# Optimization experiments

Hardware: AMD Instinct MI355X
Metric: run time of the kernel (lower is better)

## Reference

```python
import jax, jax.numpy as jnp
import numpy as np

B, N, D, K = 8, 200000, 16, 512
MAX_CP = K  # upper bound on number of condensation points per event
ATTR_W, REPL_W, BG_W = 1.0, 1.0, 2.0


def setup_inputs() -> dict:
    key = jax.random.key(0)
    k1, k2, k3 = jax.random.split(key, 3)
    beta = jax.random.normal(k1, (B, N, 1), jnp.float32)
    embed = jax.random.normal(k2, (B, N, D), jnp.float32)
    r = jax.random.randint(k3, (B, N), 0, K + 8)
    slice_id = jnp.where(r < K, r, -1).astype(jnp.int32)

    def _first_occ(sid_b):
        fg = sid_b >= 0
        seg = jnp.where(fg, sid_b, K)
        fi = jax.ops.segment_min(jnp.where(fg, jnp.arange(N), N), seg, num_segments=K + 1)[:K]
        present = fi < N
        return jnp.clip(fi, 0, N - 1), present

    fi, pres = jax.vmap(_first_occ)(slice_id)
    # exactly one condensation point per present instance (its first hit)
    is_cp = jnp.zeros((B, N), jnp.int32).at[jnp.arange(B)[:, None], fi].max(pres.astype(jnp.int32))
    return {"beta": beta, "embed": embed, "slice_id": slice_id, "is_cp": is_cp}


def _per_event(beta_b, emb_b, sid, cp):
    # beta_b:[N], emb_b:[N,D], sid:[N] int, cp:[N] int
    fg = sid >= 0
    bg = ~fg
    seg = jnp.where(fg, sid, K)            # background -> dummy segment K
    sid_c = jnp.clip(sid, 0, K - 1)
    counts = jax.ops.segment_sum(fg.astype(jnp.float32), seg, num_segments=K + 1)[:K]
    present = counts > 0
    cp_fg = (cp == 1) & fg
    cp_cnt = jax.ops.segment_sum(cp_fg.astype(jnp.float32), seg, num_segments=K + 1)[:K]
    valid = present & (cp_cnt == 1)        # instances entering the CE term

    # per-instance cross-entropy: lse(beta over instance hits) - beta[cp]
    beta_m = jnp.where(fg, beta_b, -jnp.inf)
    m = jax.ops.segment_max(beta_m, seg, num_segments=K + 1)[:K]
    m_safe = jnp.where(jnp.isfinite(m), m, 0.0)
    e = jnp.where(fg, jnp.exp(beta_b - m_safe[sid_c]), 0.0)
    sumexp = jax.ops.segment_sum(e, seg, num_segments=K + 1)[:K]
    lse = m_safe + jnp.log(jnp.maximum(sumexp, 1e-30))
    cp_beta = jax.ops.segment_sum(jnp.where(cp_fg, beta_b, 0.0), seg, num_segments=K + 1)[:K]
    ce = jnp.where(valid, lse - cp_beta, 0.0)
    slice_count = jnp.sum(valid)
    beta_loss = jnp.sum(ce) / jnp.maximum(slice_count, 1)

    # background beta penalty
    nbg = jnp.sum(bg)
    bg_mean = jnp.sum(jnp.where(bg, jax.nn.sigmoid(beta_b), 0.0)) / jnp.maximum(nbg, 1)
    beta_loss = beta_loss + jnp.where(nbg > 0, BG_W * bg_mean, 0.0)

    # attraction: per instance, mean squared distance of hits to its first cp embedding
    idx = jnp.where(cp_fg, jnp.arange(N), N)
    fi = jax.ops.segment_min(idx, seg, num_segments=K + 1)[:K]
    has_cp = present & (cp_cnt >= 1)
    cp_emb = emb_b[jnp.clip(fi, 0, N - 1)]          # [K,D]
    ref = cp_emb[sid_c]                              # [N,D] gather per hit
    d = jnp.where(fg, jnp.sum((emb_b - ref) ** 2, axis=-1), 0.0)
    dsum = jax.ops.segment_sum(d, seg, num_segments=K + 1)[:K]
    attr = ATTR_W * jnp.sum(jnp.where(has_cp, dsum / jnp.maximum(counts, 1.0), 0.0))

    # repulsion: pairwise exp(-dist^2) over ALL cp hits (diagonal included, as in torch .mean())
    cp_all = cp == 1
    ncp = jnp.sum(cp_all)
    order = jnp.argsort(jnp.where(cp_all, 0, 1))     # stable: cps first, by index
    topidx = order[:MAX_CP]
    vmask = cp_all[topidx]
    ce2 = emb_b[topidx]                               # [MAX_CP, D]
    dist2 = jnp.sum((ce2[:, None, :] - ce2[None, :, :]) ** 2, axis=-1)
    w = vmask[:, None] & vmask[None, :]
    rep_sum = jnp.sum(jnp.where(w, jnp.exp(-dist2), 0.0))
    rep = jnp.where(ncp > 1, REPL_W * rep_sum / jnp.maximum(ncp * ncp, 1), 0.0)

    loss_b = beta_loss + attr + rep
    include = slice_count > 0
    return loss_b, beta_loss, attr, rep, include


def _forward(beta, embed, slice_id, is_cp):
    loss_b, bl, al, rl, inc = jax.vmap(_per_event)(beta[..., 0], embed, slice_id, is_cp)
    incf = inc.astype(loss_b.dtype)
    count = jnp.sum(incf)
    denom = jnp.maximum(count, 1.0)
    total = jnp.where(count > 0, jnp.sum(loss_b * incf) / denom, 0.0)
    beta_log = jnp.sum(bl * incf) / denom
    attr_log = jnp.sum(al * incf) / denom
    repl_log = jnp.sum(rl * incf) / denom
    return total, beta_log, attr_log, repl_log


def reference(beta, embed, slice_id, is_cp):
    return _forward(beta, embed, slice_id, is_cp)
```

## Files before the change

kernel.cpp:

```cpp
#include <hip/hip_runtime.h>
#include <math.h>

#define Bb 8
#define Nn 200000
#define Dd 16
#define Kk 512

__global__ __launch_bounds__(256) void k_init(int* packed, float* cpb, float* se,
                                              int* fi, float* ds,
                                              int* nbg, float* sig, int* cpc, float* rep) {
  int i = blockIdx.x * 256 + threadIdx.x;
  if (i < Bb * Kk) { packed[i] = 0; cpb[i] = 0.f; se[i] = 0.f; fi[i] = Nn; ds[i] = 0.f; }
  if (i < Bb) { nbg[i] = 0; sig[i] = 0.f; cpc[i] = 0; rep[i] = 0.f; }
}

__global__ __launch_bounds__(256) void k_pass1(const float* __restrict__ beta,
                                               const int* __restrict__ sid,
                                               const int* __restrict__ cp,
                                               int* packed, float* cp_beta_g, float* sumexp_g,
                                               int* fi_g, int* nbg, float* sig,
                                               int* cp_count, int* cp_idx) {
  const int b = blockIdx.y;
  __shared__ int   s_cnt[Kk];
  __shared__ float s_cb[Kk];
  __shared__ float s_se[Kk];
  __shared__ int   s_fi[Kk];
  __shared__ int   s_nbg;
  __shared__ float s_sig;
  for (int k = threadIdx.x; k < Kk; k += 256) { s_cnt[k] = 0; s_cb[k] = 0.f; s_se[k] = 0.f; s_fi[k] = Nn; }
  if (threadIdx.x == 0) { s_nbg = 0; s_sig = 0.f; }
  __syncthreads();

  const int NV = Nn / 4;
  const int nchunks = gridDim.x;
  const int chunk = (NV + nchunks - 1) / nchunks;
  const int start = blockIdx.x * chunk;
  const int end = min(start + chunk, NV);
  const size_t base = (size_t)b * Nn;
  const int4*   sid4  = (const int4*)(sid + base);
  const int4*   cp4   = (const int4*)(cp + base);
  const float4* beta4 = (const float4*)(beta + base);

  int lnbg = 0; float lsig = 0.f;
  for (int v = start + threadIdx.x; v < end; v += 256) {
    int4 s4 = sid4[v];
    int4 c4 = cp4[v];
    float4 b4 = beta4[v];
    int ss[4] = {s4.x, s4.y, s4.z, s4.w};
    int cc[4] = {c4.x, c4.y, c4.z, c4.w};
    float bb[4] = {b4.x, b4.y, b4.z, b4.w};
    #pragma unroll
    for (int t = 0; t < 4; t++) {
      int s = ss[t], c = cc[t];
      float bv = bb[t];
      int n = v * 4 + t;
      if (s >= 0) {
        atomicAdd(&s_cnt[s], 1 + ((c == 1) ? (1 << 20) : 0));
        atomicAdd(&s_se[s], __expf(bv));
        if (c == 1) {
          atomicAdd(&s_cb[s], bv);
          atomicMin(&s_fi[s], n);
        }
      } else {
        lnbg++; lsig += 1.f / (1.f + __expf(-bv));
      }
      if (c == 1) {
        int pos = atomicAdd(&cp_count[b], 1);
        if (pos < 512) cp_idx[b * 512 + pos] = n;
      }
    }
  }
  if (lnbg) { atomicAdd(&s_nbg, lnbg); atomicAdd(&s_sig, lsig); }
  __syncthreads();

  for (int k = threadIdx.x; k < Kk; k += 256) {
    int c = s_cnt[k];
    if (c) {
      atomicAdd(&packed[b * Kk + k], c);
      atomicAdd(&sumexp_g[b * Kk + k], s_se[k]);
      float cb = s_cb[k]; if (cb != 0.f) atomicAdd(&cp_beta_g[b * Kk + k], cb);
      int f = s_fi[k];    if (f < Nn)    atomicMin(&fi_g[b * Kk + k], f);
    }
  }
  if (threadIdx.x == 0 && s_nbg) { atomicAdd(&nbg[b], s_nbg); atomicAdd(&sig[b], s_sig); }
}

__global__ __launch_bounds__(256) void k_gather(const float* __restrict__ emb,
                                                const int* __restrict__ fi_g,
                                                const int* __restrict__ cp_count,
                                                const int* __restrict__ cp_idx,
                                                float* ref_emb, float* cp_emb) {
  int i = blockIdx.x * 256 + threadIdx.x;
  const int total = Bb * Kk * Dd;
  if (i < total) {
    int b = i / (Kk * Dd);
    int rem = i % (Kk * Dd);
    int k = rem / Dd, d = rem % Dd;
    int f = fi_g[b * Kk + k]; if (f > Nn - 1) f = Nn - 1;
    ref_emb[i] = emb[((size_t)b * Nn + f) * Dd + d];
  } else {
    int j = i - total;
    if (j < Bb * 512 * Dd) {
      int b = j / (512 * Dd);
      int rem = j % (512 * Dd);
      int idx = rem / Dd, d = rem % Dd;
      int nc = cp_count[b]; if (nc > 512) nc = 512;
      if (idx < nc) {
        int n = cp_idx[b * 512 + idx];
        cp_emb[j] = emb[((size_t)b * Nn + n) * Dd + d];
      }
    }
  }
}

__global__ __launch_bounds__(256) void k_pass2(const int* __restrict__ sid,
                                               const float* __restrict__ emb,
                                               const float* __restrict__ ref_emb,
                                               float* dsum_g) {
  const int b = blockIdx.y;
  __shared__ float4 s_ref4[Kk * 5];
  __shared__ float s_d[Kk];
  {
    const float4* src = (const float4*)(ref_emb + (size_t)b * Kk * Dd);
    for (int i = threadIdx.x; i < Kk * 4; i += 256) {
      int k = i >> 2, j = i & 3;
      s_ref4[k * 5 + j] = src[i];
    }
  }
  for (int k = threadIdx.x; k < Kk; k += 256) s_d[k] = 0.f;
  __syncthreads();

  const int nchunks = gridDim.x;
  const int chunk = (Nn + nchunks - 1) / nchunks;
  const int start = blockIdx.x * chunk;
  const int end = min(start + chunk, Nn);
  const size_t base = (size_t)b * Nn;

  for (int n = start + threadIdx.x; n < end; n += 256) {
    int s = sid[base + n];
    if (s >= 0) {
      const float4* e4 = (const float4*)(emb + (base + (size_t)n) * Dd);
      float4 a0 = e4[0], a1 = e4[1], a2 = e4[2], a3 = e4[3];
      const float4* r4 = &s_ref4[s * 5];
      float4 r0 = r4[0], r1 = r4[1], r2 = r4[2], r3 = r4[3];
      float d = 0.f, df;
      df = a0.x - r0.x; d = fmaf(df, df, d);
      df = a0.y - r0.y; d = fmaf(df, df, d);
      df = a0.z - r0.z; d = fmaf(df, df, d);
      df = a0.w - r0.w; d = fmaf(df, df, d);
      df = a1.x - r1.x; d = fmaf(df, df, d);
      df = a1.y - r1.y; d = fmaf(df, df, d);
      df = a1.z - r1.z; d = fmaf(df, df, d);
      df = a1.w - r1.w; d = fmaf(df, df, d);
      df = a2.x - r2.x; d = fmaf(df, df, d);
      df = a2.y - r2.y; d = fmaf(df, df, d);
      df = a2.z - r2.z; d = fmaf(df, df, d);
      df = a2.w - r2.w; d = fmaf(df, df, d);
      df = a3.x - r3.x; d = fmaf(df, df, d);
      df = a3.y - r3.y; d = fmaf(df, df, d);
      df = a3.z - r3.z; d = fmaf(df, df, d);
      df = a3.w - r3.w; d = fmaf(df, df, d);
      atomicAdd(&s_d[s], d);
    }
  }
  __syncthreads();
  for (int k = threadIdx.x; k < Kk; k += 256) {
    float v = s_d[k];
    if (v != 0.f) atomicAdd(&dsum_g[b * Kk + k], v);
  }
}

__global__ __launch_bounds__(256) void k_rep(const float* __restrict__ cp_emb,
                                             const int* __restrict__ cp_count,
                                             float* rep_acc) {
  const int b = blockIdx.y;
  int nc = cp_count[b]; if (nc > 512) nc = 512;
  __shared__ float s_e[512 * 17];
  for (int i = threadIdx.x; i < nc * Dd; i += 256) {
    int r = i >> 4, d = i & 15;
    s_e[r * 17 + d] = cp_emb[(size_t)b * 512 * Dd + i];
  }
  __syncthreads();

  const int rows = 512 / gridDim.x;
  int i = blockIdx.x * rows + (threadIdx.x >> 3);
  int js = threadIdx.x & 7;
  float acc = 0.f;
  if (i < nc) {
    float e[16];
    #pragma unroll
    for (int d = 0; d < 16; d++) e[d] = s_e[i * 17 + d];
    for (int j = js; j < nc; j += 8) {
      const float* r = &s_e[j * 17];
      float dist = 0.f;
      #pragma unroll
      for (int d = 0; d < 16; d++) { float df = e[d] - r[d]; dist += df * df; }
      acc += __expf(-dist);
    }
  }
  __shared__ float s_red;
  if (threadIdx.x == 0) s_red = 0.f;
  __syncthreads();
  for (int off = 32; off; off >>= 1) acc += __shfl_down(acc, off, 64);
  if ((threadIdx.x & 63) == 0 && acc != 0.f) atomicAdd(&s_red, acc);
  __syncthreads();
  if (threadIdx.x == 0 && s_red != 0.f) atomicAdd(&rep_acc[b], s_red);
}

__global__ __launch_bounds__(512) void k_final(const int* __restrict__ packed,
                                               const float* __restrict__ cp_beta,
                                               const float* __restrict__ sumexp,
                                               const float* __restrict__ dsum,
                                               const int* __restrict__ nbg,
                                               const float* __restrict__ sig,
                                               const int* __restrict__ cp_count,
                                               const float* __restrict__ rep_acc,
                                               float* __restrict__ out) {
  const int b = threadIdx.x >> 6;
  const int lane = threadIdx.x & 63;
  float ce = 0.f, at = 0.f, sc = 0.f;
  #pragma unroll
  for (int i = 0; i < Kk / 64; i++) {
    int k = i * 64 + lane;
    int   pc = packed[b * Kk + k];
    float se = sumexp[b * Kk + k];
    float cb = cp_beta[b * Kk + k];
    float dv = dsum[b * Kk + k];
    int cnt = pc & 0xFFFFF;
    int cpc = pc >> 20;
    if (cnt > 0) {
      if (cpc == 1) { ce += __logf(fmaxf(se, 1e-30f)) - cb; sc += 1.f; }
      if (cpc >= 1) at += dv / (float)cnt;
    }
  }
  #pragma unroll
  for (int off = 32; off; off >>= 1) {
    ce += __shfl_down(ce, off, 64);
    at += __shfl_down(at, off, 64);
    sc += __shfl_down(sc, off, 64);
  }
  __shared__ float lb_s[Bb], bl_s[Bb], al_s[Bb], rl_s[Bb];
  __shared__ int inc_s[Bb];
  if (lane == 0) {
    int scb = (int)(sc + 0.5f);
    float bl = ce / (float)max(scb, 1);
    int nb = nbg[b];
    if (nb > 0) bl += 2.0f * sig[b] / (float)nb;
    int ncp = cp_count[b];
    float rl = (ncp > 1) ? rep_acc[b] / fmaxf((float)ncp * (float)ncp, 1.f) : 0.f;
    bl_s[b] = bl; al_s[b] = at; rl_s[b] = rl; lb_s[b] = bl + at + rl;
    inc_s[b] = (scb > 0) ? 1 : 0;
  }
  __syncthreads();
  if (threadIdx.x == 0) {
    float cnt = 0.f, st = 0.f, sb = 0.f, sa = 0.f, sr = 0.f;
    for (int b2 = 0; b2 < Bb; b2++) {
      if (inc_s[b2]) { cnt += 1.f; st += lb_s[b2]; sb += bl_s[b2]; sa += al_s[b2]; sr += rl_s[b2]; }
    }
    float denom = fmaxf(cnt, 1.f);
    out[0] = (cnt > 0.f) ? st / denom : 0.f;
    out[1] = sb / denom;
    out[2] = sa / denom;
    out[3] = sr / denom;
  }
}

extern "C" void kernel_launch(void* const* d_in, const int* in_sizes, int n_in,
                              void* d_out, int out_size, void* d_ws, size_t ws_size,
                              hipStream_t stream) {
  const float* beta = (const float*)d_in[0];
  const float* emb  = (const float*)d_in[1];
  const int*   sid  = (const int*)d_in[2];
  const int*   cp   = (const int*)d_in[3];
  float* out = (float*)d_out;

  char* ws = (char*)d_ws;
  size_t off = 0;
  auto alloc = [&](size_t bytes) -> void* {
    void* p = ws + off;
    off += (bytes + 255) & ~(size_t)255;
    return p;
  };
  int*   packed   = (int*)  alloc(Bb * Kk * sizeof(int));
  float* cp_beta  = (float*)alloc(Bb * Kk * sizeof(float));
  float* sumexp   = (float*)alloc(Bb * Kk * sizeof(float));
  int*   fi       = (int*)  alloc(Bb * Kk * sizeof(int));
  float* dsum     = (float*)alloc(Bb * Kk * sizeof(float));
  int*   nbg      = (int*)  alloc(Bb * sizeof(int));
  float* sig      = (float*)alloc(Bb * sizeof(float));
  int*   cp_count = (int*)  alloc(Bb * sizeof(int));
  float* rep_acc  = (float*)alloc(Bb * sizeof(float));
  int*   cp_idx   = (int*)  alloc(Bb * 512 * sizeof(int));
  float* ref_emb  = (float*)alloc(Bb * Kk * Dd * sizeof(float));
  float* cp_emb   = (float*)alloc(Bb * 512 * Dd * sizeof(float));

  k_init<<<(Bb * Kk + 255) / 256, 256, 0, stream>>>(packed, cp_beta, sumexp, fi, dsum,
                                                    nbg, sig, cp_count, rep_acc);
  k_pass1<<<dim3(64, Bb), 256, 0, stream>>>(beta, sid, cp, packed, cp_beta, sumexp, fi,
                                            nbg, sig, cp_count, cp_idx);
  k_gather<<<(2 * Bb * Kk * Dd + 255) / 256, 256, 0, stream>>>(emb, fi, cp_count, cp_idx,
                                                               ref_emb, cp_emb);
  k_pass2<<<dim3(128, Bb), 256, 0, stream>>>(sid, emb, ref_emb, dsum);
  k_rep<<<dim3(16, Bb), 256, 0, stream>>>(cp_emb, cp_count, rep_acc);
  k_final<<<1, 512, 0, stream>>>(packed, cp_beta, sumexp, dsum, nbg, sig,
                                 cp_count, rep_acc, out);
}
```

Baseline: 216.1 us.

## Fold gather kernel into pass2 and rep, vectorize pass2 over four points

Removes the separate gather kernel. Reference embeddings are loaded straight from emb at the first-hit indices inside pass2, and condensation-point embeddings inside k_rep, which saves one launch and the intermediate buffers. pass2 now processes four points per thread, using an int4 sid load and sixteen float4 embedding loads, with a mask in place of the branch for background points. Grid sizes also change (pass1 to 128 chunks, pass2 to 96). The shared reference array drops its padding, which may add LDS bank conflicts, and each thread now holds more registers.

```diff
diff --git a/kernel.cpp b/kernel.cpp
--- a/kernel.cpp
+++ b/kernel.cpp
@@ -85,64 +85,45 @@
   if (threadIdx.x == 0 && s_nbg) { atomicAdd(&nbg[b], s_nbg); atomicAdd(&sig[b], s_sig); }
 }
 
-__global__ __launch_bounds__(256) void k_gather(const float* __restrict__ emb,
-                                                const int* __restrict__ fi_g,
-                                                const int* __restrict__ cp_count,
-                                                const int* __restrict__ cp_idx,
-                                                float* ref_emb, float* cp_emb) {
-  int i = blockIdx.x * 256 + threadIdx.x;
-  const int total = Bb * Kk * Dd;
-  if (i < total) {
-    int b = i / (Kk * Dd);
-    int rem = i % (Kk * Dd);
-    int k = rem / Dd, d = rem % Dd;
-    int f = fi_g[b * Kk + k]; if (f > Nn - 1) f = Nn - 1;
-    ref_emb[i] = emb[((size_t)b * Nn + f) * Dd + d];
-  } else {
-    int j = i - total;
-    if (j < Bb * 512 * Dd) {
-      int b = j / (512 * Dd);
-      int rem = j % (512 * Dd);
-      int idx = rem / Dd, d = rem % Dd;
-      int nc = cp_count[b]; if (nc > 512) nc = 512;
-      if (idx < nc) {
-        int n = cp_idx[b * 512 + idx];
-        cp_emb[j] = emb[((size_t)b * Nn + n) * Dd + d];
-      }
-    }
-  }
-}
-
 __global__ __launch_bounds__(256) void k_pass2(const int* __restrict__ sid,
                                                const float* __restrict__ emb,
-                                               const float* __restrict__ ref_emb,
+                                               const int* __restrict__ fi_g,
                                                float* dsum_g) {
   const int b = blockIdx.y;
-  __shared__ float4 s_ref4[Kk * 5];
+  __shared__ float4 s_ref4[Kk * 4];
   __shared__ float s_d[Kk];
-  {
-    const float4* src = (const float4*)(ref_emb + (size_t)b * Kk * Dd);
-    for (int i = threadIdx.x; i < Kk * 4; i += 256) {
-      int k = i >> 2, j = i & 3;
-      s_ref4[k * 5 + j] = src[i];
-    }
-  }
-  for (int k = threadIdx.x; k < Kk; k += 256) s_d[k] = 0.f;
-  __syncthreads();
-
+  for (int k = threadIdx.x; k < Kk; k += 256) {
+    int f = fi_g[b * Kk + k]; if (f > Nn - 1) f = Nn - 1;
+    const float4* src = (const float4*)(emb + ((size_t)b * Nn + f) * Dd);
+    #pragma unroll
+    for (int j = 0; j < 4; j++) s_ref4[k * 4 + j] = src[j];
+    s_d[k] = 0.f;
+  }
+  __syncthreads();
+
+  const int NV = Nn / 4;
   const int nchunks = gridDim.x;
-  const int chunk = (Nn + nchunks - 1) / nchunks;
+  const int chunk = (NV + nchunks - 1) / nchunks;
   const int start = blockIdx.x * chunk;
-  const int end = min(start + chunk, Nn);
+  const int end = min(start + chunk, NV);
   const size_t base = (size_t)b * Nn;
-
-  for (int n = start + threadIdx.x; n < end; n += 256) {
-    int s = sid[base + n];
-    if (s >= 0) {
-      const float4* e4 = (const float4*)(emb + (base + (size_t)n) * Dd);
-      float4 a0 = e4[0], a1 = e4[1], a2 = e4[2], a3 = e4[3];
-      const float4* r4 = &s_ref4[s * 5];
+  const int4* sid4 = (const int4*)(sid + base);
+
+  for (int v = start + threadIdx.x; v < end; v += 256) {
+    int4 s4 = sid4[v];
+    const float4* e4 = (const float4*)(emb + (base + (size_t)v * 4) * Dd);
+    float4 a[16];
+    #pragma unroll
+    for (int t = 0; t < 16; t++) a[t] = e4[t];
+    int ss[4] = {s4.x, s4.y, s4.z, s4.w};
+    #pragma unroll
+    for (int t = 0; t < 4; t++) {
+      int s = ss[t];
+      float msk = (s >= 0) ? 1.f : 0.f;
+      int sc = (s < 0) ? 0 : s;
+      const float4* r4 = &s_ref4[sc * 4];
       float4 r0 = r4[0], r1 = r4[1], r2 = r4[2], r3 = r4[3];
+      float4 a0 = a[t*4+0], a1 = a[t*4+1], a2 = a[t*4+2], a3 = a[t*4+3];
       float d = 0.f, df;
       df = a0.x - r0.x; d = fmaf(df, df, d);
       df = a0.y - r0.y; d = fmaf(df, df, d);
@@ -160,7 +141,7 @@
       df = a3.y - r3.y; d = fmaf(df, df, d);
       df = a3.z - r3.z; d = fmaf(df, df, d);
       df = a3.w - r3.w; d = fmaf(df, df, d);
-      atomicAdd(&s_d[s], d);
+      atomicAdd(&s_d[sc], d * msk);
     }
   }
   __syncthreads();
@@ -170,15 +151,21 @@
   }
 }
 
-__global__ __launch_bounds__(256) void k_rep(const float* __restrict__ cp_emb,
+__global__ __launch_bounds__(256) void k_rep(const float* __restrict__ emb,
+                                             const int* __restrict__ cp_idx,
                                              const int* __restrict__ cp_count,
                                              float* rep_acc) {
   const int b = blockIdx.y;
   int nc = cp_count[b]; if (nc > 512) nc = 512;
   __shared__ float s_e[512 * 17];
-  for (int i = threadIdx.x; i < nc * Dd; i += 256) {
-    int r = i >> 4, d = i & 15;
-    s_e[r * 17 + d] = cp_emb[(size_t)b * 512 * Dd + i];
+  for (int i = threadIdx.x; i < nc * 4; i += 256) {
+    int r = i >> 2, j = i & 3;
+    int n = cp_idx[b * 512 + r];
+    float4 v = ((const float4*)(emb + ((size_t)b * Nn + n) * Dd))[j];
+    s_e[r * 17 + j * 4 + 0] = v.x;
+    s_e[r * 17 + j * 4 + 1] = v.y;
+    s_e[r * 17 + j * 4 + 2] = v.z;
+    s_e[r * 17 + j * 4 + 3] = v.w;
   }
   __syncthreads();
 
@@ -291,17 +278,13 @@
   int*   cp_count = (int*)  alloc(Bb * sizeof(int));
   float* rep_acc  = (float*)alloc(Bb * sizeof(float));
   int*   cp_idx   = (int*)  alloc(Bb * 512 * sizeof(int));
-  float* ref_emb  = (float*)alloc(Bb * Kk * Dd * sizeof(float));
-  float* cp_emb   = (float*)alloc(Bb * 512 * Dd * sizeof(float));
 
   k_init<<<(Bb * Kk + 255) / 256, 256, 0, stream>>>(packed, cp_beta, sumexp, fi, dsum,
                                                     nbg, sig, cp_count, rep_acc);
-  k_pass1<<<dim3(64, Bb), 256, 0, stream>>>(beta, sid, cp, packed, cp_beta, sumexp, fi,
-                                            nbg, sig, cp_count, cp_idx);
-  k_gather<<<(2 * Bb * Kk * Dd + 255) / 256, 256, 0, stream>>>(emb, fi, cp_count, cp_idx,
-                                                               ref_emb, cp_emb);
-  k_pass2<<<dim3(128, Bb), 256, 0, stream>>>(sid, emb, ref_emb, dsum);
-  k_rep<<<dim3(16, Bb), 256, 0, stream>>>(cp_emb, cp_count, rep_acc);
+  k_pass1<<<dim3(128, Bb), 256, 0, stream>>>(beta, sid, cp, packed, cp_beta, sumexp, fi,
+                                             nbg, sig, cp_count, cp_idx);
+  k_pass2<<<dim3(96, Bb), 256, 0, stream>>>(sid, emb, fi, dsum);
+  k_rep<<<dim3(16, Bb), 256, 0, stream>>>(emb, cp_idx, cp_count, rep_acc);
   k_final<<<1, 512, 0, stream>>>(packed, cp_beta, sumexp, dsum, nbg, sig,
                                  cp_count, rep_acc, out);
 }
```

Result: no change. 218.5 us (+1.1%).
